# Optimization experiments

Hardware: AMD Instinct MI355X
Metric: run time of the kernel (lower is better)

The kernel has to match this reference:

```python
import jax, jax.numpy as jnp
import numpy as np

D = 512       # d_model
L = 4         # num_layers
NH = 4        # nhead (fixed in __init__)
HD = D // NH
FF = 2 * D    # dim_feedforward = d_model*2
A = 32        # action_dim
B = 1024
STEPS = 64
SF_TH = 2.0   # sf_threshold
ALPHA = 2.0   # ATan surrogate width


@jax.custom_vjp
def spike(v):
    # Heaviside spike; surrogate gradient defined below (standard SNN practice)
    return (v > 0.0).astype(v.dtype)

def _spike_fwd(v):
    return spike(v), v

def _spike_bwd(v, g):
    sg = ALPHA / (2.0 * (1.0 + (jnp.pi / 2.0 * ALPHA * v) ** 2))
    return (g * sg,)

spike.defvjp(_spike_fwd, _spike_bwd)


def layer_norm(x, g, b):
    m = jnp.mean(x, axis=-1, keepdims=True)
    v = jnp.var(x, axis=-1, keepdims=True)
    return (x - m) / jnp.sqrt(v + 1e-5) * g + b


def setup_inputs() -> dict:
    key = jax.random.key(0)
    ks = jax.random.split(key, 24)
    w = lambda k, shape: jax.random.normal(k, shape, jnp.float32) * 0.02
    return {
        'initial_state': jax.random.normal(ks[0], (B, D), jnp.float32),
        'action_sequence': jax.random.normal(ks[1], (B, STEPS, A), jnp.float32),
        # action encoder
        'Wa': w(ks[2], (A, D)), 'ba': jnp.zeros((D,), jnp.float32),
        # per-layer SFormerBlock params, stacked on leading L dim
        'ln1_g': jnp.ones((L, D), jnp.float32), 'ln1_b': jnp.zeros((L, D), jnp.float32),
        'Wq': w(ks[3], (L, D, D)), 'bq': jnp.zeros((L, D), jnp.float32),
        'Wk': w(ks[4], (L, D, D)), 'bk': jnp.zeros((L, D), jnp.float32),
        'Wv': w(ks[5], (L, D, D)), 'bv': jnp.zeros((L, D), jnp.float32),
        'Wo': w(ks[6], (L, D, D)), 'bo': jnp.zeros((L, D), jnp.float32),
        'ln2_g': jnp.ones((L, D), jnp.float32), 'ln2_b': jnp.zeros((L, D), jnp.float32),
        'Wf1': w(ks[7], (L, D, FF)), 'bf1': jnp.zeros((L, FF), jnp.float32),
        'Wf2': w(ks[8], (L, FF, D)), 'bf2': jnp.zeros((L, D), jnp.float32),
        # transition AdaptiveLIFNeuron per-feature threshold
        'lif_th': jnp.ones((D,), jnp.float32),
        # reward head
        'Wr': w(ks[9], (D, 1)), 'br': jnp.zeros((1,), jnp.float32),
    }


def reference(initial_state, action_sequence, Wa, ba, ln1_g, ln1_b, Wq, bq, Wk, bk, Wv, bv, Wo, bo, ln2_g, ln2_b, Wf1, bf1, Wf2, bf2, lif_th, Wr, br):
    scale = 1.0 / jnp.sqrt(jnp.asarray(HD, jnp.float32))

    def block(x, l):
        # x: [B, 1, D]
        h = layer_norm(x, ln1_g[l], ln1_b[l])
        b_ = x.shape[0]
        q = (h @ Wq[l] + bq[l]).reshape(b_, 1, NH, HD)
        k = (h @ Wk[l] + bk[l]).reshape(b_, 1, NH, HD)
        v = (h @ Wv[l] + bv[l]).reshape(b_, 1, NH, HD)
        scores = jnp.einsum('bqhd,bkhd->bhqk', q, k) * scale
        attn = jax.nn.softmax(scores, axis=-1)
        o = jnp.einsum('bhqk,bkhd->bqhd', attn, v).reshape(b_, 1, D)
        x = x + o @ Wo[l] + bo[l]
        h2 = layer_norm(x, ln2_g[l], ln2_b[l])
        # spiking FFN: heaviside at sf_threshold with surrogate grad
        x = x + spike(h2 @ Wf1[l] + bf1[l] - SF_TH) @ Wf2[l] + bf2[l]
        return x

    def step(state, a):
        # predict_next_step
        x = state + a @ Wa + ba            # [B, D]
        x = x[:, None, :]                  # [B, 1, D]
        for l in range(L):
            x = block(x, l)
        x = x[:, 0, :]
        next_state = spike(x - lif_th)     # transition_lif (single-step LIF: v = input)
        reward = next_state @ Wr + br      # [B, 1]
        return next_state, (next_state, reward)

    acts = jnp.swapaxes(action_sequence, 0, 1)  # [Steps, B, A]
    final_state, (S, R) = jax.lax.scan(step, initial_state, acts)
    states = jnp.swapaxes(S, 0, 1)    # [B, Steps, D]
    rewards = jnp.swapaxes(R, 0, 1)   # [B, Steps, 1]
    return states, rewards, final_state
```

## Files before the change

### kernel.cpp

```cpp
#include <hip/hip_runtime.h>

#define D_ 512
#define FF_ 1024
#define L_ 4
#define A_ 32
#define B_ 1024
#define STEPS_ 64
#define RB_ 0.0625f

typedef __attribute__((ext_vector_type(8))) short bf16x8;
typedef __attribute__((ext_vector_type(4))) float f32x4;
#define MFMA16(a,b,c) __builtin_amdgcn_mfma_f32_16x16x32_bf16(a,b,c,0,0,0)

__device__ __forceinline__ unsigned rne16(float f) {
    unsigned u = __float_as_uint(f);
    return (u + 0x7fffu + ((u >> 16) & 1u)) >> 16;
}
__device__ __forceinline__ float fb(unsigned hu) { return __uint_as_float(hu << 16); }

__global__ __launch_bounds__(256) void wvo_kernel(
    const float* __restrict__ Wv, const float* __restrict__ Wo,
    unsigned* __restrict__ Whi, unsigned* __restrict__ Wlo)
{
    __shared__ float wvt[16][D_];
    int bx  = blockIdx.x;
    int l   = bx >> 6;
    int rem = bx & 63;
    int k0  = (rem >> 1) * 16;
    int n   = (rem & 1) * 256 + threadIdx.x;

    const float* wvbase = Wv + (size_t)l * D_ * D_ + (size_t)k0 * D_;
    for (int idx = threadIdx.x; idx < 16 * D_; idx += 256)
        wvt[idx >> 9][idx & (D_ - 1)] = wvbase[idx];
    __syncthreads();

    float acc[16];
#pragma unroll
    for (int kk = 0; kk < 16; ++kk) acc[kk] = 0.f;

    const float* wop = Wo + (size_t)l * D_ * D_ + n;
    for (int m = 0; m < D_; m += 4) {
        float w0 = wop[(m + 0) * D_];
        float w1 = wop[(m + 1) * D_];
        float w2 = wop[(m + 2) * D_];
        float w3 = wop[(m + 3) * D_];
#pragma unroll
        for (int kk = 0; kk < 16; ++kk) {
            float4 wv4 = *(const float4*)&wvt[kk][m];
            acc[kk] += wv4.x * w0 + wv4.y * w1 + wv4.z * w2 + wv4.w * w3;
        }
    }
    int nt = n >> 4, ln15 = n & 15;
    int kkblk = k0 >> 5;
    int gbase = (k0 & 31) >> 3;
#pragma unroll
    for (int gi = 0; gi < 2; ++gi) {
        int lane_s = ((gbase + gi) << 4) | ln15;
        size_t fbase = ((((size_t)l * 32 + nt) * 16 + kkblk) * 64 + lane_s) * 4;
#pragma unroll
        for (int jp = 0; jp < 4; ++jp) {
            float v0 = acc[gi * 8 + jp * 2], v1 = acc[gi * 8 + jp * 2 + 1];
            unsigned h0 = rne16(v0), h1 = rne16(v1);
            Whi[fbase + jp] = h0 | (h1 << 16);
            float r0 = v0 - fb(h0), r1 = v1 - fb(h1);
            Wlo[fbase + jp] = rne16(r0) | (rne16(r1) << 16);
        }
    }
}

__global__ __launch_bounds__(256) void bvo_kernel(
    const float* __restrict__ bv, const float* __restrict__ bo,
    const float* __restrict__ Wo, float* __restrict__ bvo)
{
    int l = blockIdx.x >> 1;
    int n = (blockIdx.x & 1) * 256 + threadIdx.x;
    float acc = bo[l * D_ + n];
    const float* wop = Wo + (size_t)l * D_ * D_ + n;
    const float* bvp = bv + l * D_;
    for (int m = 0; m < D_; ++m) acc += bvp[m] * wop[m * D_];
    bvo[l * D_ + n] = acc;
}

__global__ __launch_bounds__(64) void packwf1_kernel(
    const float* __restrict__ Wf1, unsigned* __restrict__ Pf)
{
    int bid = blockIdx.x;
    int lane = threadIdx.x;
    int l  = bid >> 10;
    int nt = (bid >> 4) & 63;
    int kk = bid & 15;
    int krow = kk * 32 + (lane >> 4) * 8;
    int n    = nt * 16 + (lane & 15);
    const float* src = Wf1 + ((size_t)l * D_ + krow) * FF_ + n;
    unsigned o[4];
#pragma unroll
    for (int jp = 0; jp < 4; ++jp) {
        unsigned a = rne16(src[(2 * jp) * FF_]);
        unsigned b = rne16(src[(2 * jp + 1) * FF_]);
        o[jp] = a | (b << 16);
    }
    size_t fbase = (((size_t)(l * 64 + nt) * 16 + kk) * 64 + lane) * 4;
    Pf[fbase + 0] = o[0]; Pf[fbase + 1] = o[1];
    Pf[fbase + 2] = o[2]; Pf[fbase + 3] = o[3];
}

__device__ __forceinline__ void layer_norm_frag(
    float (*xb)[D_], unsigned* __restrict__ afrag,
    const float* __restrict__ g, const float* __restrict__ bt,
    float (*red)[4][2], int sg, int r)
{
    int c = 2 * r;
    float v0 = xb[sg][c], v1 = xb[sg][c + 1];
    float s  = v0 + v1;
    float ss = v0 * v0 + v1 * v1;
#pragma unroll
    for (int m = 1; m < 64; m <<= 1) {
        s  += __shfl_xor(s, m);
        ss += __shfl_xor(ss, m);
    }
    if ((r & 63) == 0) { red[sg][r >> 6][0] = s; red[sg][r >> 6][1] = ss; }
    __syncthreads();
    float S  = red[sg][0][0] + red[sg][1][0] + red[sg][2][0] + red[sg][3][0];
    float SS = red[sg][0][1] + red[sg][1][1] + red[sg][2][1] + red[sg][3][1];
    float mean = S * (1.f / 512.f);
    float var  = SS * (1.f / 512.f) - mean * mean;
    float rstd = 1.0f / sqrtf(var + 1e-5f);
    float h0 = (v0 - mean) * rstd * g[c]     + bt[c];
    float h1 = (v1 - mean) * rstd * g[c + 1] + bt[c + 1];
    unsigned u0 = rne16(h0), u1 = rne16(h1);
    float l0 = h0 - fb(u0), l1 = h1 - fb(u1);
    int kk = c >> 5, grp = (c & 31) >> 3, jp = (c & 7) >> 1;
    afrag[(kk * 64 + ((grp << 4) | sg))       * 4 + jp] = u0 | (u1 << 16);
    afrag[(kk * 64 + ((grp << 4) | (sg + 4))) * 4 + jp] = rne16(l0) | (rne16(l1) << 16);
    __syncthreads();
}

__global__ __launch_bounds__(1024) void smain(
    const float* __restrict__ init_state,
    const float* __restrict__ acts,
    const float* __restrict__ Wa,  const float* __restrict__ ba,
    const float* __restrict__ ln1g, const float* __restrict__ ln1b,
    const float* __restrict__ ln2g, const float* __restrict__ ln2b,
    const float* __restrict__ Wf1, const float* __restrict__ bf1,
    const float* __restrict__ Wf2, const float* __restrict__ bf2,
    const float* __restrict__ lifth,
    const float* __restrict__ Wr,  const float* __restrict__ br,
    const unsigned* __restrict__ Whi, const unsigned* __restrict__ Wlo,
    const unsigned* __restrict__ Pf, const float* __restrict__ bvo,
    float* __restrict__ out_states, float* __restrict__ out_rewards,
    float* __restrict__ out_final)
{
    __shared__ __align__(16) unsigned afrag[16 * 64 * 4];
    __shared__ __align__(16) float xb[4][D_];
    __shared__ __align__(16) float sb[4][D_];
    __shared__ float areg[4][A_];
    __shared__ float red[4][4][2];
    __shared__ float rr[16];
    __shared__ int   fire_cnt, resc_cnt;
    __shared__ int   fire_list[256];
    __shared__ int   rescue_list[64];

    const int tid  = threadIdx.x;
    const int sg   = tid >> 8;
    const int r    = tid & 255;
    const int wv   = tid >> 6;
    const int lane = tid & 63;
    const int b    = blockIdx.x * 4 + sg;

    sb[sg][r]       = init_state[(size_t)b * D_ + r];
    sb[sg][r + 256] = init_state[(size_t)b * D_ + r + 256];
#pragma unroll
    for (int z = 0; z < 4; ++z) afrag[tid + z * 1024] = 0;
    __syncthreads();

    for (int t = 0; t < STEPS_; ++t) {
        if (tid < 128) {
            int sg2 = tid >> 5, j = tid & 31;
            areg[sg2][j] = acts[((size_t)(blockIdx.x * 4 + sg2)) * (STEPS_ * A_) + t * A_ + j];
        }
        __syncthreads();

        {
            float2 xv;
            xv.x = sb[sg][2 * r]     + ba[2 * r];
            xv.y = sb[sg][2 * r + 1] + ba[2 * r + 1];
#pragma unroll
            for (int j = 0; j < A_; ++j) {
                float av = areg[sg][j];
                float2 w = *(const float2*)(Wa + j * D_ + 2 * r);
                xv.x += av * w.x; xv.y += av * w.y;
            }
            xb[sg][2 * r] = xv.x; xb[sg][2 * r + 1] = xv.y;
        }
        __syncthreads();

        for (int l = 0; l < L_; ++l) {
            layer_norm_frag(xb, afrag, ln1g + l * D_, ln1b + l * D_, red, sg, r);

            {
                const bf16x8* Ah = (const bf16x8*)afrag;
                const size_t lb = (size_t)l * 32 * 16 * 64;
                const bf16x8* BH = (const bf16x8*)Whi + lb;
                const bf16x8* BL = (const bf16x8*)Wlo + lb;
                const int nt0 = 2 * wv, nt1 = nt0 + 1;
                f32x4 c1a = {0.f,0.f,0.f,0.f}, c2a = c1a, c1b = c1a, c2b = c1a;
#pragma unroll 4
                for (int kk = 0; kk < 16; ++kk) {
                    bf16x8 a  = Ah[kk * 64 + lane];
                    bf16x8 h0 = BH[(nt0 * 16 + kk) * 64 + lane];
                    bf16x8 g0 = BL[(nt0 * 16 + kk) * 64 + lane];
                    bf16x8 h1 = BH[(nt1 * 16 + kk) * 64 + lane];
                    bf16x8 g1 = BL[(nt1 * 16 + kk) * 64 + lane];
                    c1a = MFMA16(a, h0, c1a); c2a = MFMA16(a, g0, c2a);
                    c1b = MFMA16(a, h1, c1b); c2b = MFMA16(a, g1, c2b);
                }
#pragma unroll
                for (int s = 0; s < 4; ++s) {
                    float pa = c1a[s] + c2a[s]; float qa = __shfl(pa, (lane & 15) + 16);
                    float pb = c1b[s] + c2b[s]; float qb = __shfl(pb, (lane & 15) + 16);
                    if (lane < 16) {
                        int ca = nt0 * 16 + lane, cb = nt1 * 16 + lane;
                        xb[s][ca] += pa + qa + bvo[l * D_ + ca];
                        xb[s][cb] += pb + qb + bvo[l * D_ + cb];
                    }
                }
            }
            __syncthreads();

            if (tid == 0) { fire_cnt = 0; resc_cnt = 0; }

            layer_norm_frag(xb, afrag, ln2g + l * D_, ln2b + l * D_, red, sg, r);

            {
                const bf16x8* Ah = (const bf16x8*)afrag;
                const bf16x8* PB = (const bf16x8*)Pf + (size_t)l * 64 * 16 * 64;
                const int m0 = 4 * wv;
                f32x4 p0 = {0.f,0.f,0.f,0.f}, p1 = p0, p2 = p0, p3 = p0;
#pragma unroll 4
                for (int kk = 0; kk < 16; ++kk) {
                    bf16x8 a  = Ah[kk * 64 + lane];
                    bf16x8 b0 = PB[((m0 + 0) * 16 + kk) * 64 + lane];
                    bf16x8 b1 = PB[((m0 + 1) * 16 + kk) * 64 + lane];
                    bf16x8 b2 = PB[((m0 + 2) * 16 + kk) * 64 + lane];
                    bf16x8 b3 = PB[((m0 + 3) * 16 + kk) * 64 + lane];
                    p0 = MFMA16(a, b0, p0); p1 = MFMA16(a, b1, p1);
                    p2 = MFMA16(a, b2, p2); p3 = MFMA16(a, b3, p3);
                }
                const float* bf1g = bf1 + l * FF_;
#pragma unroll
                for (int s = 0; s < 4; ++s) {
                    float v0 = p0[s]; float w0 = __shfl(v0, (lane & 15) + 16);
                    float v1 = p1[s]; float w1 = __shfl(v1, (lane & 15) + 16);
                    float v2 = p2[s]; float w2 = __shfl(v2, (lane & 15) + 16);
                    float v3 = p3[s]; float w3 = __shfl(v3, (lane & 15) + 16);
                    if (lane < 16) {
#pragma unroll
                        for (int q = 0; q < 4; ++q) {
                            float sum = (q == 0) ? v0 + w0 : (q == 1) ? v1 + w1
                                       : (q == 2) ? v2 + w2 : v3 + w3;
                            int n = (m0 + q) * 16 + lane;
                            float pr = sum + bf1g[n] - 2.0f;
                            if (pr > RB_) {
                                int idx = atomicAdd(&fire_cnt, 1);
                                if (idx < 256) fire_list[idx] = (s << 12) | n;
                            } else if (pr > -RB_) {
                                int idx = atomicAdd(&resc_cnt, 1);
                                if (idx < 64) rescue_list[idx] = (s << 12) | n;
                            }
                        }
                    }
                }
            }
            __syncthreads();

            {
                int rc = resc_cnt; if (rc > 64) rc = 64;
                for (int e = 0; e < rc; ++e) {
                    int ent = rescue_list[e];
                    int i = ent >> 12, n = ent & 4095;
                    float p = 0.f;
                    if (tid < D_) {
                        int k = tid;
                        int kk = k >> 5, grp = (k & 31) >> 3, jp = (k & 7) >> 1;
                        unsigned whi = afrag[(kk * 64 + ((grp << 4) | i))       * 4 + jp];
                        unsigned wlo = afrag[(kk * 64 + ((grp << 4) | (i + 4))) * 4 + jp];
                        unsigned sh = (k & 1) ? 16 : 0;
                        float h = fb((whi >> sh) & 0xffffu) + fb((wlo >> sh) & 0xffffu);
                        p = h * Wf1[((size_t)l * D_ + k) * FF_ + n];
                    }
#pragma unroll
                    for (int m = 1; m < 64; m <<= 1) p += __shfl_xor(p, m);
                    if ((tid & 63) == 0) rr[tid >> 6] = p;
                    __syncthreads();
                    if (tid == 0) {
                        float dot = 0.f;
#pragma unroll
                        for (int w = 0; w < 8; ++w) dot += rr[w];
                        float pre = dot + bf1[l * FF_ + n] - 2.0f;
                        if (pre > 0.f) {
                            int idx = atomicAdd(&fire_cnt, 1);
                            if (idx < 256) fire_list[idx] = ent;
                        }
                    }
                    __syncthreads();
                }
            }

            {
                int cnt = fire_cnt; if (cnt > 256) cnt = 256;
                if (cnt > 0) {
                    for (int e = 0; e < cnt; ++e) {
                        int ent = fire_list[e];
                        int i = ent >> 12, n = ent & 4095;
                        if (tid < D_) xb[i][tid] += Wf2[(size_t)l * (FF_ * D_) + (size_t)n * D_ + tid];
                    }
                    __syncthreads();
                }
                xb[sg][r]       += bf2[l * D_ + r];
                xb[sg][r + 256] += bf2[l * D_ + r + 256];
            }
            __syncthreads();
        }

        {
            float x0 = xb[sg][r], x1 = xb[sg][r + 256];
            float s0 = (x0 > lifth[r])       ? 1.0f : 0.0f;
            float s1 = (x1 > lifth[r + 256]) ? 1.0f : 0.0f;
            sb[sg][r] = s0; sb[sg][r + 256] = s1;
            size_t so = ((size_t)b * STEPS_ + t) * D_;
            out_states[so + r]       = s0;
            out_states[so + r + 256] = s1;

            float rs = s0 * Wr[r] + s1 * Wr[r + 256];
#pragma unroll
            for (int m = 1; m < 64; m <<= 1) rs += __shfl_xor(rs, m);
            if ((r & 63) == 0) red[sg][r >> 6][0] = rs;
            __syncthreads();
            if (r == 0)
                out_rewards[(size_t)b * STEPS_ + t] =
                    red[sg][0][0] + red[sg][1][0] + red[sg][2][0] + red[sg][3][0] + br[0];
        }
        __syncthreads();
    }

    out_final[(size_t)b * D_ + r]       = sb[sg][r];
    out_final[(size_t)b * D_ + r + 256] = sb[sg][r + 256];
}

extern "C" void kernel_launch(void* const* d_in, const int* in_sizes, int n_in,
                              void* d_out, int out_size, void* d_ws, size_t ws_size,
                              hipStream_t stream) {
    (void)in_sizes; (void)n_in; (void)out_size; (void)ws_size;
    const float* init_state = (const float*)d_in[0];
    const float* acts  = (const float*)d_in[1];
    const float* Wa    = (const float*)d_in[2];
    const float* ba    = (const float*)d_in[3];
    const float* ln1g  = (const float*)d_in[4];
    const float* ln1b  = (const float*)d_in[5];
    const float* Wv    = (const float*)d_in[10];
    const float* bv    = (const float*)d_in[11];
    const float* Wo    = (const float*)d_in[12];
    const float* bo    = (const float*)d_in[13];
    const float* ln2g  = (const float*)d_in[14];
    const float* ln2b  = (const float*)d_in[15];
    const float* Wf1   = (const float*)d_in[16];
    const float* bf1   = (const float*)d_in[17];
    const float* Wf2   = (const float*)d_in[18];
    const float* bf2   = (const float*)d_in[19];
    const float* lifth = (const float*)d_in[20];
    const float* Wr    = (const float*)d_in[21];
    const float* br    = (const float*)d_in[22];

    unsigned* Whi = (unsigned*)d_ws;
    unsigned* Wlo = Whi + 524288;
    unsigned* Pf  = Wlo + 524288;
    float*    bvo = (float*)(Pf + 1048576);

    float* out         = (float*)d_out;
    float* out_states  = out;
    float* out_rewards = out + (size_t)B_ * STEPS_ * D_;
    float* out_final   = out_rewards + (size_t)B_ * STEPS_;

    wvo_kernel<<<dim3(256), dim3(256), 0, stream>>>(Wv, Wo, Whi, Wlo);
    bvo_kernel<<<dim3(8),   dim3(256), 0, stream>>>(bv, bo, Wo, bvo);
    packwf1_kernel<<<dim3(4096), dim3(64), 0, stream>>>(Wf1, Pf);
    smain<<<dim3(256), dim3(1024), 0, stream>>>(
        init_state, acts, Wa, ba, ln1g, ln1b, ln2g, ln2b,
        Wf1, bf1, Wf2, bf2, lifth, Wr, br, Whi, Wlo, Pf, bvo,
        out_states, out_rewards, out_final);
}
```

Measured before the change: 7.827 ms.

## Process eight batch rows per block to reuse weight fragments across two tiles

Each block now handles eight batch rows as two 4-row MFMA A-tiles. Every weight fragment loaded from global memory feeds both tiles, so total weight traffic from L2 is halved and the grid drops to 128 blocks. The carried spike state is kept as bytes in shared memory, and output stores use nontemporal hints. In exchange only half as many blocks run, and the per-block serial work (layer norms, fire and rescue handling) doubles. The shared 256-entry fire list now has to hold entries for eight rows, which could overflow.

```diff
diff --git a/kernel.cpp b/kernel.cpp
--- a/kernel.cpp
+++ b/kernel.cpp
@@ -104,13 +104,14 @@
     Pf[fbase + 2] = o[2]; Pf[fbase + 3] = o[3];
 }
 
-__device__ __forceinline__ void layer_norm_frag(
-    float (*xb)[D_], unsigned* __restrict__ afrag,
+__device__ __forceinline__ void layer_norm_frag8(
+    const float* __restrict__ xbase,
+    unsigned* __restrict__ afrag,
     const float* __restrict__ g, const float* __restrict__ bt,
     float (*red)[4][2], int sg, int r)
 {
     int c = 2 * r;
-    float v0 = xb[sg][c], v1 = xb[sg][c + 1];
+    float v0 = xbase[sg * D_ + c], v1 = xbase[sg * D_ + c + 1];
     float s  = v0 + v1;
     float ss = v0 * v0 + v1 * v1;
 #pragma unroll
@@ -129,13 +130,13 @@
     float h1 = (v1 - mean) * rstd * g[c + 1] + bt[c + 1];
     unsigned u0 = rne16(h0), u1 = rne16(h1);
     float l0 = h0 - fb(u0), l1 = h1 - fb(u1);
-    int kk = c >> 5, grp = (c & 31) >> 3, jp = (c & 7) >> 1;
-    afrag[(kk * 64 + ((grp << 4) | sg))       * 4 + jp] = u0 | (u1 << 16);
-    afrag[(kk * 64 + ((grp << 4) | (sg + 4))) * 4 + jp] = rne16(l0) | (rne16(l1) << 16);
+    int kk = c >> 5, gg = (c & 31) >> 3, jp = (c & 7) >> 1;
+    afrag[(kk * 64 + ((gg << 4) | sg))       * 4 + jp] = u0 | (u1 << 16);
+    afrag[(kk * 64 + ((gg << 4) | (sg + 4))) * 4 + jp] = rne16(l0) | (rne16(l1) << 16);
     __syncthreads();
 }
 
-__global__ __launch_bounds__(1024) void smain(
+__global__ __launch_bounds__(1024, 4) void smain(
     const float* __restrict__ init_state,
     const float* __restrict__ acts,
     const float* __restrict__ Wa,  const float* __restrict__ ba,
@@ -150,10 +151,10 @@
     float* __restrict__ out_states, float* __restrict__ out_rewards,
     float* __restrict__ out_final)
 {
-    __shared__ __align__(16) unsigned afrag[16 * 64 * 4];
-    __shared__ __align__(16) float xb[4][D_];
-    __shared__ __align__(16) float sb[4][D_];
-    __shared__ float areg[4][A_];
+    __shared__ __align__(16) unsigned afrag2[2][16 * 64 * 4];
+    __shared__ __align__(16) float xb[8 * D_];
+    __shared__ unsigned char sb8[8][D_];
+    __shared__ float areg[8][A_];
     __shared__ float red[4][4][2];
     __shared__ float rr[16];
     __shared__ int   fire_cnt, resc_cnt;
@@ -165,63 +166,81 @@
     const int r    = tid & 255;
     const int wv   = tid >> 6;
     const int lane = tid & 63;
-    const int b    = blockIdx.x * 4 + sg;
-
-    sb[sg][r]       = init_state[(size_t)b * D_ + r];
-    sb[sg][r + 256] = init_state[(size_t)b * D_ + r + 256];
-#pragma unroll
-    for (int z = 0; z < 4; ++z) afrag[tid + z * 1024] = 0;
+    const int b0   = blockIdx.x * 8;
+
+    {
+        unsigned* az = (unsigned*)afrag2;
+#pragma unroll
+        for (int z = 0; z < 8; ++z) az[tid + z * 1024] = 0;
+    }
     __syncthreads();
 
     for (int t = 0; t < STEPS_; ++t) {
-        if (tid < 128) {
-            int sg2 = tid >> 5, j = tid & 31;
-            areg[sg2][j] = acts[((size_t)(blockIdx.x * 4 + sg2)) * (STEPS_ * A_) + t * A_ + j];
+        if (tid < 256) {
+            int s2 = tid >> 5, j = tid & 31;
+            areg[s2][j] = acts[(size_t)(b0 + s2) * (STEPS_ * A_) + t * A_ + j];
         }
         __syncthreads();
 
-        {
+#pragma unroll
+        for (int gsel = 0; gsel < 2; ++gsel) {
+            int s = gsel * 4 + sg;
+            float2 st;
+            if (t == 0) st = *(const float2*)&init_state[(size_t)(b0 + s) * D_ + 2 * r];
+            else        st = make_float2((float)sb8[s][2 * r], (float)sb8[s][2 * r + 1]);
             float2 xv;
-            xv.x = sb[sg][2 * r]     + ba[2 * r];
-            xv.y = sb[sg][2 * r + 1] + ba[2 * r + 1];
+            xv.x = st.x + ba[2 * r];
+            xv.y = st.y + ba[2 * r + 1];
 #pragma unroll
             for (int j = 0; j < A_; ++j) {
-                float av = areg[sg][j];
-                float2 w = *(const float2*)(Wa + j * D_ + 2 * r);
-                xv.x += av * w.x; xv.y += av * w.y;
+                float av = areg[s][j];
+                float2 w2 = *(const float2*)(Wa + j * D_ + 2 * r);
+                xv.x += av * w2.x; xv.y += av * w2.y;
             }
-            xb[sg][2 * r] = xv.x; xb[sg][2 * r + 1] = xv.y;
+            xb[s * D_ + 2 * r] = xv.x; xb[s * D_ + 2 * r + 1] = xv.y;
         }
         __syncthreads();
 
         for (int l = 0; l < L_; ++l) {
-            layer_norm_frag(xb, afrag, ln1g + l * D_, ln1b + l * D_, red, sg, r);
+            layer_norm_frag8(xb,           afrag2[0], ln1g + l * D_, ln1b + l * D_, red, sg, r);
+            layer_norm_frag8(xb + 4 * D_,  afrag2[1], ln1g + l * D_, ln1b + l * D_, red, sg, r);
 
             {
-                const bf16x8* Ah = (const bf16x8*)afrag;
-                const size_t lb = (size_t)l * 32 * 16 * 64;
+                const bf16x8* A0 = (const bf16x8*)(afrag2[0]);
+                const bf16x8* A1 = (const bf16x8*)(afrag2[1]);
+                const size_t lb = (size_t)l * (32 * 16 * 64);
                 const bf16x8* BH = (const bf16x8*)Whi + lb;
                 const bf16x8* BL = (const bf16x8*)Wlo + lb;
                 const int nt0 = 2 * wv, nt1 = nt0 + 1;
-                f32x4 c1a = {0.f,0.f,0.f,0.f}, c2a = c1a, c1b = c1a, c2b = c1a;
-#pragma unroll 4
+                f32x4 z = {0.f, 0.f, 0.f, 0.f};
+                f32x4 cA1a = z, cA2a = z, cA1b = z, cA2b = z;
+                f32x4 cB1a = z, cB2a = z, cB1b = z, cB2b = z;
+#pragma unroll 2
                 for (int kk = 0; kk < 16; ++kk) {
-                    bf16x8 a  = Ah[kk * 64 + lane];
+                    bf16x8 aA = A0[kk * 64 + lane];
+                    bf16x8 aB = A1[kk * 64 + lane];
                     bf16x8 h0 = BH[(nt0 * 16 + kk) * 64 + lane];
                     bf16x8 g0 = BL[(nt0 * 16 + kk) * 64 + lane];
                     bf16x8 h1 = BH[(nt1 * 16 + kk) * 64 + lane];
                     bf16x8 g1 = BL[(nt1 * 16 + kk) * 64 + lane];
-                    c1a = MFMA16(a, h0, c1a); c2a = MFMA16(a, g0, c2a);
-                    c1b = MFMA16(a, h1, c1b); c2b = MFMA16(a, g1, c2b);
-                }
+                    cA1a = MFMA16(aA, h0, cA1a); cA2a = MFMA16(aA, g0, cA2a);
+                    cA1b = MFMA16(aA, h1, cA1b); cA2b = MFMA16(aA, g1, cA2b);
+                    cB1a = MFMA16(aB, h0, cB1a); cB2a = MFMA16(aB, g0, cB2a);
+                    cB1b = MFMA16(aB, h1, cB1b); cB2b = MFMA16(aB, g1, cB2b);
+                }
+                const float* bvog = bvo + l * D_;
 #pragma unroll
                 for (int s = 0; s < 4; ++s) {
-                    float pa = c1a[s] + c2a[s]; float qa = __shfl(pa, (lane & 15) + 16);
-                    float pb = c1b[s] + c2b[s]; float qb = __shfl(pb, (lane & 15) + 16);
+                    float pa = cA1a[s] + cA2a[s]; float qa = __shfl(pa, (lane & 15) + 16);
+                    float pb = cA1b[s] + cA2b[s]; float qb = __shfl(pb, (lane & 15) + 16);
+                    float pc = cB1a[s] + cB2a[s]; float qc = __shfl(pc, (lane & 15) + 16);
+                    float pd = cB1b[s] + cB2b[s]; float qd = __shfl(pd, (lane & 15) + 16);
                     if (lane < 16) {
                         int ca = nt0 * 16 + lane, cb = nt1 * 16 + lane;
-                        xb[s][ca] += pa + qa + bvo[l * D_ + ca];
-                        xb[s][cb] += pb + qb + bvo[l * D_ + cb];
+                        xb[s * D_ + ca]       += pa + qa + bvog[ca];
+                        xb[s * D_ + cb]       += pb + qb + bvog[cb];
+                        xb[(s + 4) * D_ + ca] += pc + qc + bvog[ca];
+                        xb[(s + 4) * D_ + cb] += pd + qd + bvog[cb];
                     }
                 }
             }
@@ -229,43 +248,63 @@
 
             if (tid == 0) { fire_cnt = 0; resc_cnt = 0; }
 
-            layer_norm_frag(xb, afrag, ln2g + l * D_, ln2b + l * D_, red, sg, r);
+            layer_norm_frag8(xb,          afrag2[0], ln2g + l * D_, ln2b + l * D_, red, sg, r);
+            layer_norm_frag8(xb + 4 * D_, afrag2[1], ln2g + l * D_, ln2b + l * D_, red, sg, r);
 
             {
-                const bf16x8* Ah = (const bf16x8*)afrag;
-                const bf16x8* PB = (const bf16x8*)Pf + (size_t)l * 64 * 16 * 64;
+                const bf16x8* A0 = (const bf16x8*)(afrag2[0]);
+                const bf16x8* A1 = (const bf16x8*)(afrag2[1]);
+                const bf16x8* PB = (const bf16x8*)Pf + (size_t)l * (64 * 16 * 64);
                 const int m0 = 4 * wv;
-                f32x4 p0 = {0.f,0.f,0.f,0.f}, p1 = p0, p2 = p0, p3 = p0;
-#pragma unroll 4
+                f32x4 z = {0.f, 0.f, 0.f, 0.f};
+                f32x4 pA0 = z, pA1 = z, pA2 = z, pA3 = z;
+                f32x4 pB0 = z, pB1 = z, pB2 = z, pB3 = z;
+#pragma unroll 2
                 for (int kk = 0; kk < 16; ++kk) {
-                    bf16x8 a  = Ah[kk * 64 + lane];
+                    bf16x8 aA = A0[kk * 64 + lane];
+                    bf16x8 aB = A1[kk * 64 + lane];
                     bf16x8 b0 = PB[((m0 + 0) * 16 + kk) * 64 + lane];
                     bf16x8 b1 = PB[((m0 + 1) * 16 + kk) * 64 + lane];
                     bf16x8 b2 = PB[((m0 + 2) * 16 + kk) * 64 + lane];
                     bf16x8 b3 = PB[((m0 + 3) * 16 + kk) * 64 + lane];
-                    p0 = MFMA16(a, b0, p0); p1 = MFMA16(a, b1, p1);
-                    p2 = MFMA16(a, b2, p2); p3 = MFMA16(a, b3, p3);
+                    pA0 = MFMA16(aA, b0, pA0); pA1 = MFMA16(aA, b1, pA1);
+                    pA2 = MFMA16(aA, b2, pA2); pA3 = MFMA16(aA, b3, pA3);
+                    pB0 = MFMA16(aB, b0, pB0); pB1 = MFMA16(aB, b1, pB1);
+                    pB2 = MFMA16(aB, b2, pB2); pB3 = MFMA16(aB, b3, pB3);
                 }
                 const float* bf1g = bf1 + l * FF_;
 #pragma unroll
                 for (int s = 0; s < 4; ++s) {
-                    float v0 = p0[s]; float w0 = __shfl(v0, (lane & 15) + 16);
-                    float v1 = p1[s]; float w1 = __shfl(v1, (lane & 15) + 16);
-                    float v2 = p2[s]; float w2 = __shfl(v2, (lane & 15) + 16);
-                    float v3 = p3[s]; float w3 = __shfl(v3, (lane & 15) + 16);
+                    float vA0 = pA0[s]; float wA0 = __shfl(vA0, (lane & 15) + 16);
+                    float vA1 = pA1[s]; float wA1 = __shfl(vA1, (lane & 15) + 16);
+                    float vA2 = pA2[s]; float wA2 = __shfl(vA2, (lane & 15) + 16);
+                    float vA3 = pA3[s]; float wA3 = __shfl(vA3, (lane & 15) + 16);
+                    float vB0 = pB0[s]; float wB0 = __shfl(vB0, (lane & 15) + 16);
+                    float vB1 = pB1[s]; float wB1 = __shfl(vB1, (lane & 15) + 16);
+                    float vB2 = pB2[s]; float wB2 = __shfl(vB2, (lane & 15) + 16);
+                    float vB3 = pB3[s]; float wB3 = __shfl(vB3, (lane & 15) + 16);
                     if (lane < 16) {
+                        float sumA[4] = {vA0 + wA0, vA1 + wA1, vA2 + wA2, vA3 + wA3};
+                        float sumB[4] = {vB0 + wB0, vB1 + wB1, vB2 + wB2, vB3 + wB3};
 #pragma unroll
                         for (int q = 0; q < 4; ++q) {
-                            float sum = (q == 0) ? v0 + w0 : (q == 1) ? v1 + w1
-                                       : (q == 2) ? v2 + w2 : v3 + w3;
                             int n = (m0 + q) * 16 + lane;
-                            float pr = sum + bf1g[n] - 2.0f;
-                            if (pr > RB_) {
+                            float bb = bf1g[n] - 2.0f;
+                            float prA = sumA[q] + bb;
+                            if (prA > RB_) {
                                 int idx = atomicAdd(&fire_cnt, 1);
                                 if (idx < 256) fire_list[idx] = (s << 12) | n;
-                            } else if (pr > -RB_) {
+                            } else if (prA > -RB_) {
                                 int idx = atomicAdd(&resc_cnt, 1);
                                 if (idx < 64) rescue_list[idx] = (s << 12) | n;
+                            }
+                            float prB = sumB[q] + bb;
+                            if (prB > RB_) {
+                                int idx = atomicAdd(&fire_cnt, 1);
+                                if (idx < 256) fire_list[idx] = ((s + 4) << 12) | n;
+                            } else if (prB > -RB_) {
+                                int idx = atomicAdd(&resc_cnt, 1);
+                                if (idx < 64) rescue_list[idx] = ((s + 4) << 12) | n;
                             }
                         }
                     }
@@ -278,13 +317,15 @@
                 for (int e = 0; e < rc; ++e) {
                     int ent = rescue_list[e];
                     int i = ent >> 12, n = ent & 4095;
+                    int tile = i >> 2, ri = i & 3;
                     float p = 0.f;
                     if (tid < D_) {
                         int k = tid;
-                        int kk = k >> 5, grp = (k & 31) >> 3, jp = (k & 7) >> 1;
-                        unsigned whi = afrag[(kk * 64 + ((grp << 4) | i))       * 4 + jp];
-                        unsigned wlo = afrag[(kk * 64 + ((grp << 4) | (i + 4))) * 4 + jp];
-                        unsigned sh = (k & 1) ? 16 : 0;
+                        int kk = k >> 5, gg = (k & 31) >> 3, jp = (k & 7) >> 1;
+                        unsigned sh = (k & 1) ? 16u : 0u;
+                        const unsigned* af = afrag2[tile];
+                        unsigned whi = af[(kk * 64 + ((gg << 4) | ri))       * 4 + jp];
+                        unsigned wlo = af[(kk * 64 + ((gg << 4) | (ri + 4))) * 4 + jp];
                         float h = fb((whi >> sh) & 0xffffu) + fb((wlo >> sh) & 0xffffu);
                         p = h * Wf1[((size_t)l * D_ + k) * FF_ + n];
                     }
@@ -295,7 +336,7 @@
                     if (tid == 0) {
                         float dot = 0.f;
 #pragma unroll
-                        for (int w = 0; w < 8; ++w) dot += rr[w];
+                        for (int w2 = 0; w2 < 16; ++w2) dot += rr[w2];
                         float pre = dot + bf1[l * FF_ + n] - 2.0f;
                         if (pre > 0.f) {
                             int idx = atomicAdd(&fire_cnt, 1);
@@ -308,28 +349,32 @@
 
             {
                 int cnt = fire_cnt; if (cnt > 256) cnt = 256;
-                if (cnt > 0) {
-                    for (int e = 0; e < cnt; ++e) {
-                        int ent = fire_list[e];
-                        int i = ent >> 12, n = ent & 4095;
-                        if (tid < D_) xb[i][tid] += Wf2[(size_t)l * (FF_ * D_) + (size_t)n * D_ + tid];
-                    }
-                    __syncthreads();
-                }
-                xb[sg][r]       += bf2[l * D_ + r];
-                xb[sg][r + 256] += bf2[l * D_ + r + 256];
+                for (int e = 0; e < cnt; ++e) {
+                    int ent = fire_list[e];
+                    int i = ent >> 12, n = ent & 4095;
+                    if (tid < D_) xb[i * D_ + tid] += Wf2[(size_t)l * (FF_ * D_) + (size_t)n * D_ + tid];
+                }
+                if (cnt > 0) __syncthreads();
+#pragma unroll
+                for (int gsel = 0; gsel < 2; ++gsel) {
+                    int s = gsel * 4 + sg;
+                    xb[s * D_ + r]       += bf2[l * D_ + r];
+                    xb[s * D_ + r + 256] += bf2[l * D_ + r + 256];
+                }
             }
             __syncthreads();
         }
 
-        {
-            float x0 = xb[sg][r], x1 = xb[sg][r + 256];
+        for (int gsel = 0; gsel < 2; ++gsel) {
+            int s = gsel * 4 + sg;
+            float x0 = xb[s * D_ + r], x1 = xb[s * D_ + r + 256];
             float s0 = (x0 > lifth[r])       ? 1.0f : 0.0f;
             float s1 = (x1 > lifth[r + 256]) ? 1.0f : 0.0f;
-            sb[sg][r] = s0; sb[sg][r + 256] = s1;
-            size_t so = ((size_t)b * STEPS_ + t) * D_;
-            out_states[so + r]       = s0;
-            out_states[so + r + 256] = s1;
+            sb8[s][r]       = (unsigned char)s0;
+            sb8[s][r + 256] = (unsigned char)s1;
+            size_t so = ((size_t)(b0 + s) * STEPS_ + t) * D_;
+            __builtin_nontemporal_store(s0, &out_states[so + r]);
+            __builtin_nontemporal_store(s1, &out_states[so + r + 256]);
 
             float rs = s0 * Wr[r] + s1 * Wr[r + 256];
 #pragma unroll
@@ -337,14 +382,19 @@
             if ((r & 63) == 0) red[sg][r >> 6][0] = rs;
             __syncthreads();
             if (r == 0)
-                out_rewards[(size_t)b * STEPS_ + t] =
-                    red[sg][0][0] + red[sg][1][0] + red[sg][2][0] + red[sg][3][0] + br[0];
-        }
-        __syncthreads();
-    }
-
-    out_final[(size_t)b * D_ + r]       = sb[sg][r];
-    out_final[(size_t)b * D_ + r + 256] = sb[sg][r + 256];
+                __builtin_nontemporal_store(
+                    red[sg][0][0] + red[sg][1][0] + red[sg][2][0] + red[sg][3][0] + br[0],
+                    &out_rewards[(size_t)(b0 + s) * STEPS_ + t]);
+            __syncthreads();
+        }
+    }
+
+#pragma unroll
+    for (int gsel = 0; gsel < 2; ++gsel) {
+        int s = gsel * 4 + sg;
+        __builtin_nontemporal_store((float)sb8[s][r],       &out_final[(size_t)(b0 + s) * D_ + r]);
+        __builtin_nontemporal_store((float)sb8[s][r + 256], &out_final[(size_t)(b0 + s) * D_ + r + 256]);
+    }
 }
 
 extern "C" void kernel_launch(void* const* d_in, const int* in_sizes, int n_in,
@@ -384,7 +434,7 @@
     wvo_kernel<<<dim3(256), dim3(256), 0, stream>>>(Wv, Wo, Whi, Wlo);
     bvo_kernel<<<dim3(8),   dim3(256), 0, stream>>>(bv, bo, Wo, bvo);
     packwf1_kernel<<<dim3(4096), dim3(64), 0, stream>>>(Wf1, Pf);
-    smain<<<dim3(256), dim3(1024), 0, stream>>>(
+    smain<<<dim3(128), dim3(1024), 0, stream>>>(
         init_state, acts, Wa, ba, ln1g, ln1b, ln2g, ln2b,
         Wf1, bf1, Wf2, bf2, lifth, Wr, br, Whi, Wlo, Pf, bvo,
         out_states, out_rewards, out_final);
```

Measured after the change: 8.586 ms. 1.1x slower.

## Software-pipeline weight fragment loads in MFMA loops and use nontemporal output stores

Applied to the files above, without the earlier changes.

Both MFMA k-loops now prefetch the weight fragments four k-steps ahead into register ring buffers, so global-load latency overlaps with MFMA issue. Output stores for states, rewards and the final state become nontemporal to avoid polluting cache. The launch bounds also gain a min-blocks hint of 4. The prefetch adds register pressure, and the occupancy hint may force spills at 1024 threads per block.

```diff
diff --git a/kernel.cpp b/kernel.cpp
--- a/kernel.cpp
+++ b/kernel.cpp
@@ -135,7 +135,7 @@
     __syncthreads();
 }
 
-__global__ __launch_bounds__(1024) void smain(
+__global__ __launch_bounds__(1024, 4) void smain(
     const float* __restrict__ init_state,
     const float* __restrict__ acts,
     const float* __restrict__ Wa,  const float* __restrict__ ba,
@@ -204,13 +204,25 @@
                 const bf16x8* BL = (const bf16x8*)Wlo + lb;
                 const int nt0 = 2 * wv, nt1 = nt0 + 1;
                 f32x4 c1a = {0.f,0.f,0.f,0.f}, c2a = c1a, c1b = c1a, c2b = c1a;
-#pragma unroll 4
+                bf16x8 sh0[4], sg0[4], sh1[4], sg1[4];
+#pragma unroll
+                for (int p = 0; p < 4; ++p) {
+                    sh0[p] = BH[(nt0 * 16 + p) * 64 + lane];
+                    sg0[p] = BL[(nt0 * 16 + p) * 64 + lane];
+                    sh1[p] = BH[(nt1 * 16 + p) * 64 + lane];
+                    sg1[p] = BL[(nt1 * 16 + p) * 64 + lane];
+                }
+#pragma unroll
                 for (int kk = 0; kk < 16; ++kk) {
+                    const int st = kk & 3;
                     bf16x8 a  = Ah[kk * 64 + lane];
-                    bf16x8 h0 = BH[(nt0 * 16 + kk) * 64 + lane];
-                    bf16x8 g0 = BL[(nt0 * 16 + kk) * 64 + lane];
-                    bf16x8 h1 = BH[(nt1 * 16 + kk) * 64 + lane];
-                    bf16x8 g1 = BL[(nt1 * 16 + kk) * 64 + lane];
+                    bf16x8 h0 = sh0[st], g0 = sg0[st], h1 = sh1[st], g1 = sg1[st];
+                    if (kk < 12) {
+                        sh0[st] = BH[(nt0 * 16 + kk + 4) * 64 + lane];
+                        sg0[st] = BL[(nt0 * 16 + kk + 4) * 64 + lane];
+                        sh1[st] = BH[(nt1 * 16 + kk + 4) * 64 + lane];
+                        sg1[st] = BL[(nt1 * 16 + kk + 4) * 64 + lane];
+                    }
                     c1a = MFMA16(a, h0, c1a); c2a = MFMA16(a, g0, c2a);
                     c1b = MFMA16(a, h1, c1b); c2b = MFMA16(a, g1, c2b);
                 }
@@ -236,13 +248,25 @@
                 const bf16x8* PB = (const bf16x8*)Pf + (size_t)l * 64 * 16 * 64;
                 const int m0 = 4 * wv;
                 f32x4 p0 = {0.f,0.f,0.f,0.f}, p1 = p0, p2 = p0, p3 = p0;
-#pragma unroll 4
+                bf16x8 s0[4], s1[4], s2[4], s3[4];
+#pragma unroll
+                for (int p = 0; p < 4; ++p) {
+                    s0[p] = PB[((m0 + 0) * 16 + p) * 64 + lane];
+                    s1[p] = PB[((m0 + 1) * 16 + p) * 64 + lane];
+                    s2[p] = PB[((m0 + 2) * 16 + p) * 64 + lane];
+                    s3[p] = PB[((m0 + 3) * 16 + p) * 64 + lane];
+                }
+#pragma unroll
                 for (int kk = 0; kk < 16; ++kk) {
+                    const int st = kk & 3;
                     bf16x8 a  = Ah[kk * 64 + lane];
-                    bf16x8 b0 = PB[((m0 + 0) * 16 + kk) * 64 + lane];
-                    bf16x8 b1 = PB[((m0 + 1) * 16 + kk) * 64 + lane];
-                    bf16x8 b2 = PB[((m0 + 2) * 16 + kk) * 64 + lane];
-                    bf16x8 b3 = PB[((m0 + 3) * 16 + kk) * 64 + lane];
+                    bf16x8 b0 = s0[st], b1 = s1[st], b2 = s2[st], b3 = s3[st];
+                    if (kk < 12) {
+                        s0[st] = PB[((m0 + 0) * 16 + kk + 4) * 64 + lane];
+                        s1[st] = PB[((m0 + 1) * 16 + kk + 4) * 64 + lane];
+                        s2[st] = PB[((m0 + 2) * 16 + kk + 4) * 64 + lane];
+                        s3[st] = PB[((m0 + 3) * 16 + kk + 4) * 64 + lane];
+                    }
                     p0 = MFMA16(a, b0, p0); p1 = MFMA16(a, b1, p1);
                     p2 = MFMA16(a, b2, p2); p3 = MFMA16(a, b3, p3);
                 }
@@ -328,8 +352,8 @@
             float s1 = (x1 > lifth[r + 256]) ? 1.0f : 0.0f;
             sb[sg][r] = s0; sb[sg][r + 256] = s1;
             size_t so = ((size_t)b * STEPS_ + t) * D_;
-            out_states[so + r]       = s0;
-            out_states[so + r + 256] = s1;
+            __builtin_nontemporal_store(s0, &out_states[so + r]);
+            __builtin_nontemporal_store(s1, &out_states[so + r + 256]);
 
             float rs = s0 * Wr[r] + s1 * Wr[r + 256];
 #pragma unroll
@@ -337,14 +361,15 @@
             if ((r & 63) == 0) red[sg][r >> 6][0] = rs;
             __syncthreads();
             if (r == 0)
-                out_rewards[(size_t)b * STEPS_ + t] =
-                    red[sg][0][0] + red[sg][1][0] + red[sg][2][0] + red[sg][3][0] + br[0];
+                __builtin_nontemporal_store(
+                    red[sg][0][0] + red[sg][1][0] + red[sg][2][0] + red[sg][3][0] + br[0],
+                    &out_rewards[(size_t)b * STEPS_ + t]);
         }
         __syncthreads();
     }
 
-    out_final[(size_t)b * D_ + r]       = sb[sg][r];
-    out_final[(size_t)b * D_ + r + 256] = sb[sg][r + 256];
+    __builtin_nontemporal_store(sb[sg][r],       &out_final[(size_t)b * D_ + r]);
+    __builtin_nontemporal_store(sb[sg][r + 256], &out_final[(size_t)b * D_ + r + 256]);
 }
 
 extern "C" void kernel_launch(void* const* d_in, const int* in_sizes, int n_in,
```

New measurement: 9.322 ms. 19.1% more time.

## Double-buffer weight fragments into LDS via global_load_lds in GEMM loops

Applied to the files above, without the earlier changes.

Both MFMA loops now stage each k-slice of weight fragments into a double-buffered LDS area using direct global-to-LDS loads, prefetching the next slice while the current one is consumed. Before, each wave read its fragments straight from global memory. This adds a block-wide barrier on every k iteration and 128KB of LDS. Separately, the recurrent state moves from shared memory into registers and the output writes become nontemporal stores.

```diff
diff --git a/kernel.cpp b/kernel.cpp
--- a/kernel.cpp
+++ b/kernel.cpp
@@ -17,6 +17,12 @@
     return (u + 0x7fffu + ((u >> 16) & 1u)) >> 16;
 }
 __device__ __forceinline__ float fb(unsigned hu) { return __uint_as_float(hu << 16); }
+
+__device__ __forceinline__ void gld_lds16(const unsigned* g, void* l) {
+    __builtin_amdgcn_global_load_lds(
+        (const __attribute__((address_space(1))) unsigned*)g,
+        (__attribute__((address_space(3))) unsigned*)l, 16, 0, 0);
+}
 
 __global__ __launch_bounds__(256) void wvo_kernel(
     const float* __restrict__ Wv, const float* __restrict__ Wo,
@@ -150,9 +156,9 @@
     float* __restrict__ out_states, float* __restrict__ out_rewards,
     float* __restrict__ out_final)
 {
+    __shared__ __align__(16) uint4   stage[2][4096];
     __shared__ __align__(16) unsigned afrag[16 * 64 * 4];
     __shared__ __align__(16) float xb[4][D_];
-    __shared__ __align__(16) float sb[4][D_];
     __shared__ float areg[4][A_];
     __shared__ float red[4][4][2];
     __shared__ float rr[16];
@@ -167,8 +173,8 @@
     const int lane = tid & 63;
     const int b    = blockIdx.x * 4 + sg;
 
-    sb[sg][r]       = init_state[(size_t)b * D_ + r];
-    sb[sg][r + 256] = init_state[(size_t)b * D_ + r + 256];
+    float st0 = init_state[(size_t)b * D_ + r];
+    float st1 = init_state[(size_t)b * D_ + r + 256];
 #pragma unroll
     for (int z = 0; z < 4; ++z) afrag[tid + z * 1024] = 0;
     __syncthreads();
@@ -181,39 +187,55 @@
         __syncthreads();
 
         {
-            float2 xv;
-            xv.x = sb[sg][2 * r]     + ba[2 * r];
-            xv.y = sb[sg][2 * r + 1] + ba[2 * r + 1];
+            float x0 = st0 + ba[r];
+            float x1 = st1 + ba[r + 256];
 #pragma unroll
             for (int j = 0; j < A_; ++j) {
                 float av = areg[sg][j];
-                float2 w = *(const float2*)(Wa + j * D_ + 2 * r);
-                xv.x += av * w.x; xv.y += av * w.y;
+                x0 += av * Wa[j * D_ + r];
+                x1 += av * Wa[j * D_ + r + 256];
             }
-            xb[sg][2 * r] = xv.x; xb[sg][2 * r + 1] = xv.y;
+            xb[sg][r] = x0; xb[sg][r + 256] = x1;
         }
         __syncthreads();
 
         for (int l = 0; l < L_; ++l) {
+            const unsigned* WHl = Whi + (size_t)l * (32 * 16 * 64 * 4);
+            const unsigned* WLl = Wlo + (size_t)l * (32 * 16 * 64 * 4);
+            const unsigned* Pl  = Pf  + (size_t)l * (64 * 16 * 64 * 4);
+
             layer_norm_frag(xb, afrag, ln1g + l * D_, ln1b + l * D_, red, sg, r);
 
             {
                 const bf16x8* Ah = (const bf16x8*)afrag;
-                const size_t lb = (size_t)l * 32 * 16 * 64;
-                const bf16x8* BH = (const bf16x8*)Whi + lb;
-                const bf16x8* BL = (const bf16x8*)Wlo + lb;
-                const int nt0 = 2 * wv, nt1 = nt0 + 1;
                 f32x4 c1a = {0.f,0.f,0.f,0.f}, c2a = c1a, c1b = c1a, c2b = c1a;
-#pragma unroll 4
+#define STAGE_G1(BUF, KK) do {                                               \
+    _Pragma("unroll")                                                        \
+    for (int q = 0; q < 4; ++q) {                                            \
+        int c_ = q * 16 + wv;                                                \
+        int nt_ = c_ >> 1;                                                   \
+        const unsigned* src_ = ((c_ & 1) ? WLl : WHl) +                      \
+            (((size_t)nt_ * 16 + (KK)) * 64 + lane) * 4;                     \
+        gld_lds16(src_, &stage[BUF][(size_t)c_ * 64]);                       \
+    } } while (0)
+                STAGE_G1(0, 0);
+                __syncthreads();
+#pragma unroll
                 for (int kk = 0; kk < 16; ++kk) {
+                    const int cur = kk & 1;
+                    if (kk < 15) STAGE_G1(cur ^ 1, kk + 1);
+                    const bf16x8* SB = (const bf16x8*)stage[cur];
                     bf16x8 a  = Ah[kk * 64 + lane];
-                    bf16x8 h0 = BH[(nt0 * 16 + kk) * 64 + lane];
-                    bf16x8 g0 = BL[(nt0 * 16 + kk) * 64 + lane];
-                    bf16x8 h1 = BH[(nt1 * 16 + kk) * 64 + lane];
-                    bf16x8 g1 = BL[(nt1 * 16 + kk) * 64 + lane];
+                    bf16x8 h0 = SB[(4 * wv + 0) * 64 + lane];
+                    bf16x8 g0 = SB[(4 * wv + 1) * 64 + lane];
+                    bf16x8 h1 = SB[(4 * wv + 2) * 64 + lane];
+                    bf16x8 g1 = SB[(4 * wv + 3) * 64 + lane];
                     c1a = MFMA16(a, h0, c1a); c2a = MFMA16(a, g0, c2a);
                     c1b = MFMA16(a, h1, c1b); c2b = MFMA16(a, g1, c2b);
-                }
+                    __syncthreads();
+                }
+#undef STAGE_G1
+                const int nt0 = 2 * wv, nt1 = nt0 + 1;
 #pragma unroll
                 for (int s = 0; s < 4; ++s) {
                     float pa = c1a[s] + c2a[s]; float qa = __shfl(pa, (lane & 15) + 16);
@@ -233,19 +255,33 @@
 
             {
                 const bf16x8* Ah = (const bf16x8*)afrag;
-                const bf16x8* PB = (const bf16x8*)Pf + (size_t)l * 64 * 16 * 64;
                 const int m0 = 4 * wv;
                 f32x4 p0 = {0.f,0.f,0.f,0.f}, p1 = p0, p2 = p0, p3 = p0;
-#pragma unroll 4
+#define STAGE_G2(BUF, KK) do {                                               \
+    _Pragma("unroll")                                                        \
+    for (int q = 0; q < 4; ++q) {                                            \
+        int nt_ = q * 16 + wv;                                               \
+        const unsigned* src_ = Pl +                                          \
+            (((size_t)nt_ * 16 + (KK)) * 64 + lane) * 4;                     \
+        gld_lds16(src_, &stage[BUF][(size_t)nt_ * 64]);                      \
+    } } while (0)
+                STAGE_G2(0, 0);
+                __syncthreads();
+#pragma unroll
                 for (int kk = 0; kk < 16; ++kk) {
+                    const int cur = kk & 1;
+                    if (kk < 15) STAGE_G2(cur ^ 1, kk + 1);
+                    const bf16x8* SB = (const bf16x8*)stage[cur];
                     bf16x8 a  = Ah[kk * 64 + lane];
-                    bf16x8 b0 = PB[((m0 + 0) * 16 + kk) * 64 + lane];
-                    bf16x8 b1 = PB[((m0 + 1) * 16 + kk) * 64 + lane];
-                    bf16x8 b2 = PB[((m0 + 2) * 16 + kk) * 64 + lane];
-                    bf16x8 b3 = PB[((m0 + 3) * 16 + kk) * 64 + lane];
+                    bf16x8 b0 = SB[(m0 + 0) * 64 + lane];
+                    bf16x8 b1 = SB[(m0 + 1) * 64 + lane];
+                    bf16x8 b2 = SB[(m0 + 2) * 64 + lane];
+                    bf16x8 b3 = SB[(m0 + 3) * 64 + lane];
                     p0 = MFMA16(a, b0, p0); p1 = MFMA16(a, b1, p1);
                     p2 = MFMA16(a, b2, p2); p3 = MFMA16(a, b3, p3);
-                }
+                    __syncthreads();
+                }
+#undef STAGE_G2
                 const float* bf1g = bf1 + l * FF_;
 #pragma unroll
                 for (int s = 0; s < 4; ++s) {
@@ -326,10 +362,10 @@
             float x0 = xb[sg][r], x1 = xb[sg][r + 256];
             float s0 = (x0 > lifth[r])       ? 1.0f : 0.0f;
             float s1 = (x1 > lifth[r + 256]) ? 1.0f : 0.0f;
-            sb[sg][r] = s0; sb[sg][r + 256] = s1;
+            st0 = s0; st1 = s1;
             size_t so = ((size_t)b * STEPS_ + t) * D_;
-            out_states[so + r]       = s0;
-            out_states[so + r + 256] = s1;
+            __builtin_nontemporal_store(s0, &out_states[so + r]);
+            __builtin_nontemporal_store(s1, &out_states[so + r + 256]);
 
             float rs = s0 * Wr[r] + s1 * Wr[r + 256];
 #pragma unroll
@@ -337,14 +373,15 @@
             if ((r & 63) == 0) red[sg][r >> 6][0] = rs;
             __syncthreads();
             if (r == 0)
-                out_rewards[(size_t)b * STEPS_ + t] =
-                    red[sg][0][0] + red[sg][1][0] + red[sg][2][0] + red[sg][3][0] + br[0];
+                __builtin_nontemporal_store(
+                    red[sg][0][0] + red[sg][1][0] + red[sg][2][0] + red[sg][3][0] + br[0],
+                    &out_rewards[(size_t)b * STEPS_ + t]);
         }
         __syncthreads();
     }
 
-    out_final[(size_t)b * D_ + r]       = sb[sg][r];
-    out_final[(size_t)b * D_ + r + 256] = sb[sg][r + 256];
+    __builtin_nontemporal_store(st0, &out_final[(size_t)b * D_ + r]);
+    __builtin_nontemporal_store(st1, &out_final[(size_t)b * D_ + r + 256]);
 }
 
 extern "C" void kernel_launch(void* const* d_in, const int* in_sizes, int n_in,
```

Result: slower. 18.47 ms (+136.0%).
